# Kernel tuning notes

Hardware: AMD Instinct MI355X
Metric: run time of the kernel (lower is better)

## Reference

```python
import jax, jax.numpy as jnp
import numpy as np

NTOKENS = 50257
NHID = 1024
TPC = int(np.ceil(np.sqrt(NTOKENS)))          # 225 tokens per class
NCLASSES = int(np.ceil(NTOKENS / TPC))        # 224 classes
BATCH = 2048
INITRANGE = 0.1


def setup_inputs() -> dict:
    key = jax.random.key(0)
    k1, k2, k3, k4 = jax.random.split(key, 4)
    inputs = jax.random.normal(k1, (BATCH, NHID), dtype=jnp.float32)
    labels = jax.random.randint(k2, (BATCH,), 0, NTOKENS, dtype=jnp.int32)
    W_top = jax.random.uniform(k3, (NHID, NCLASSES), dtype=jnp.float32,
                               minval=-INITRANGE, maxval=INITRANGE)
    b_top = jnp.zeros((NCLASSES,), dtype=jnp.float32)
    W_bottom = jax.random.uniform(k4, (NCLASSES, NHID, TPC), dtype=jnp.float32,
                                  minval=-INITRANGE, maxval=INITRANGE)
    b_bottom = jnp.zeros((NCLASSES, TPC), dtype=jnp.float32)
    return {"inputs": inputs, "labels": labels, "W_top": W_top, "b_top": b_top,
            "W_bottom": W_bottom, "b_bottom": b_bottom}


def reference(inputs, labels, W_top, b_top, W_bottom, b_bottom):
    # Two-level hierarchical softmax: P(word) = P(class | h) * P(word | class, h)
    batch = inputs.shape[0]
    cls = labels // TPC          # [B] class index at top level
    word = labels % TPC          # [B] word index within class

    # Top level: [B, nclasses]
    top_probs = jax.nn.softmax(inputs @ W_top + b_top, axis=1)
    p_cls = top_probs[jnp.arange(batch), cls]            # [B]

    # Bottom level: gather per-example class weights then batched matvec
    Wb = W_bottom[cls]                                    # [B, nhid, tpc]
    bb = b_bottom[cls]                                    # [B, tpc]
    bottom_logits = jnp.einsum('bd,bdk->bk', inputs, Wb) + bb
    bottom_probs = jax.nn.softmax(bottom_logits, axis=1)
    p_word = bottom_probs[jnp.arange(batch), word]        # [B]

    return p_cls * p_word
```

## Files before the change

kernel.cpp:

```cpp
#include <hip/hip_runtime.h>
#include <math.h>

#define TPC 225
#define NCLS 224
#define NHID 1024
#define BATCH 2048
#define CAP 256
#define LSTRIDE 256

__global__ __launch_bounds__(256) void hs_bucket(const int* __restrict__ labels,
                                                 int* __restrict__ bucket,
                                                 int* __restrict__ cnt) {
    __shared__ int scnt[NCLS];
    const int t = threadIdx.x;
    for (int i = t; i < NCLS; i += 256) scnt[i] = 0;
    __syncthreads();
    for (int b = t; b < BATCH; b += 256) {
        int lab = labels[b];
        int c = lab / TPC;
        int pos = atomicAdd(&scnt[c], 1);
        bucket[c * CAP + pos] = b;
    }
    __syncthreads();
    for (int i = t; i < NCLS; i += 256) cnt[i] = scnt[i];
}

__global__ __launch_bounds__(1024, 4) void hs_tlogits(const float* __restrict__ x,
                                                      const float* __restrict__ W,
                                                      float* __restrict__ tws) {
    __shared__ float red[8 * 8 * 256];
    const int t = threadIdx.x;
    const int lane = t & 63;
    const int wave = t >> 6;
    const int wr = wave & 1;
    const int wd = wave >> 1;
    const int r0 = blockIdx.x * 8;

    const float* pj[4];
#pragma unroll
    for (int j = 0; j < 4; j++) {
        int k = 64 * j + lane;
        pj[j] = W + (size_t)wd * 128 * NCLS + (k < NCLS ? k : NCLS - 1);
    }
    const float* xp[4];
#pragma unroll
    for (int rl = 0; rl < 4; rl++)
        xp[rl] = x + (size_t)(r0 + wr * 4 + rl) * NHID + wd * 128;

    float acc[4][4] = {};
    for (int dq = 0; dq < 32; ++dq) {
        float w[4][4];
#pragma unroll
        for (int di = 0; di < 4; di++)
#pragma unroll
            for (int j = 0; j < 4; j++) w[di][j] = pj[j][di * NCLS];
#pragma unroll
        for (int rl = 0; rl < 4; rl++) {
            float4 xq = *(const float4*)(xp[rl] + dq * 4);
#pragma unroll
            for (int di = 0; di < 4; di++) {
                float xv = ((const float*)&xq)[di];
#pragma unroll
                for (int j = 0; j < 4; j++)
                    acc[rl][j] = fmaf(xv, w[di][j], acc[rl][j]);
            }
        }
#pragma unroll
        for (int j = 0; j < 4; j++) pj[j] += 4 * NCLS;
    }
#pragma unroll
    for (int rl = 0; rl < 4; rl++)
#pragma unroll
        for (int j = 0; j < 4; j++)
            red[(wd * 8 + wr * 4 + rl) * 256 + 64 * j + lane] = acc[rl][j];
    __syncthreads();

    const int u = t & 255;
    for (int r = t >> 8; r < 8; r += 4) {
        if (u < NCLS) {
            float s = 0.f;
#pragma unroll
            for (int w8 = 0; w8 < 8; w8++) s += red[(w8 * 8 + r) * 256 + u];
            tws[(size_t)(r0 + r) * LSTRIDE + u] = s;
        }
    }
}

template <int RW>
__device__ __forceinline__ void bpass(const float* __restrict__ x,
                                      const float* __restrict__ wb,
                                      const int* __restrict__ bucket_c,
                                      const int base, const int n,
                                      const int lane, const int wr, const int wd,
                                      float* __restrict__ red) {
    const float* xp[RW];
#pragma unroll
    for (int rl = 0; rl < RW; rl++) {
        int idx = base + wr * RW + rl;
        int row = bucket_c[idx < n ? idx : 0];
        xp[rl] = x + (size_t)row * NHID + wd * 256;
    }
    const float* pj[4];
#pragma unroll
    for (int j = 0; j < 4; j++) {
        int k = 64 * j + lane;
        pj[j] = wb + (k < TPC ? k : TPC - 1);
    }
    float acc[RW][4] = {};
    for (int dq = 0; dq < 64; ++dq) {
        float w[4][4];
#pragma unroll
        for (int di = 0; di < 4; di++)
#pragma unroll
            for (int j = 0; j < 4; j++) w[di][j] = pj[j][di * TPC];
#pragma unroll
        for (int rl = 0; rl < RW; rl++) {
            float4 xq = *(const float4*)(xp[rl] + dq * 4);
#pragma unroll
            for (int di = 0; di < 4; di++) {
                float xv = ((const float*)&xq)[di];
#pragma unroll
                for (int j = 0; j < 4; j++)
                    acc[rl][j] = fmaf(xv, w[di][j], acc[rl][j]);
            }
        }
#pragma unroll
        for (int j = 0; j < 4; j++) pj[j] += 4 * TPC;
    }
#pragma unroll
    for (int rl = 0; rl < RW; rl++)
#pragma unroll
        for (int j = 0; j < 4; j++)
            red[(wd * 16 + wr * RW + rl) * 256 + 64 * j + lane] = acc[rl][j];
}

__global__ __launch_bounds__(1024, 4) void hs_blogits(const float* __restrict__ x,
                                                      const float* __restrict__ Wb,
                                                      const int* __restrict__ bucket,
                                                      const int* __restrict__ cnt,
                                                      float* __restrict__ bws) {
    __shared__ float red[4 * 16 * 256];
    const int c = blockIdx.x;
    const int n = cnt[c];
    if (n == 0) return;
    const int t = threadIdx.x;
    const int lane = t & 63;
    const int wave = t >> 6;
    const int wr = wave >> 2;
    const int wd = wave & 3;
    const float* wb = Wb + (size_t)c * (NHID * TPC) + (size_t)wd * 256 * TPC;
    const int* bucket_c = bucket + c * CAP;

    for (int base = 0; base < n; base += 16) {
        int m = n - base;
        if (m > 16) m = 16;
        const int RW = (m + 3) >> 2;
        if (base) __syncthreads();
        switch (RW) {
            case 1: bpass<1>(x, wb, bucket_c, base, n, lane, wr, wd, red); break;
            case 2: bpass<2>(x, wb, bucket_c, base, n, lane, wr, wd, red); break;
            case 3: bpass<3>(x, wb, bucket_c, base, n, lane, wr, wd, red); break;
            default: bpass<4>(x, wb, bucket_c, base, n, lane, wr, wd, red); break;
        }
        __syncthreads();
        const int u = t & 255;
        for (int r = t >> 8; r < m; r += 4) {
            if (u < TPC) {
                float s = 0.f;
#pragma unroll
                for (int w4 = 0; w4 < 4; w4++) s += red[(w4 * 16 + r) * 256 + u];
                int row = bucket_c[base + r];
                bws[(size_t)row * LSTRIDE + u] = s;
            }
        }
    }
}

__global__ __launch_bounds__(256) void hs_finish(const float* __restrict__ tws,
                                                 const float* __restrict__ bws,
                                                 const int* __restrict__ labels,
                                                 const float* __restrict__ b_top,
                                                 const float* __restrict__ b_bot,
                                                 float* __restrict__ out) {
    const int lane = threadIdx.x & 63;
    const int wave = threadIdx.x >> 6;
    const int row = blockIdx.x * 4 + wave;
    const int label = labels[row];
    const int c = label / TPC;
    const int word = label - c * TPC;

    float p[2];
#pragma unroll
    for (int lvl = 0; lvl < 2; lvl++) {
        const int NS = lvl ? TPC : NCLS;
        const int pick = lvl ? word : c;
        const float* lws = lvl ? bws : tws;
        const float* bias = lvl ? (b_bot + c * TPC) : b_top;
        float lg[4];
#pragma unroll
        for (int j = 0; j < 4; j++) {
            int k = lane + 64 * j;
            lg[j] = (k < NS) ? lws[(size_t)row * LSTRIDE + k] + bias[k] : -INFINITY;
        }
        float m = fmaxf(fmaxf(lg[0], lg[1]), fmaxf(lg[2], lg[3]));
#pragma unroll
        for (int off = 32; off > 0; off >>= 1) m = fmaxf(m, __shfl_xor(m, off, 64));
        float s = 0.f, pp = 0.f;
#pragma unroll
        for (int j = 0; j < 4; j++) {
            int k = lane + 64 * j;
            float e = (k < NS) ? __expf(lg[j] - m) : 0.f;
            s += e;
            if (k == pick) pp = e;
        }
#pragma unroll
        for (int off = 32; off > 0; off >>= 1) {
            s += __shfl_xor(s, off, 64);
            pp += __shfl_xor(pp, off, 64);
        }
        p[lvl] = pp / s;
    }
    if (lane == 0) out[row] = p[0] * p[1];
}

extern "C" void kernel_launch(void* const* d_in, const int* in_sizes, int n_in,
                              void* d_out, int out_size, void* d_ws, size_t ws_size,
                              hipStream_t stream) {
    const float* inputs   = (const float*)d_in[0];
    const int*   labels   = (const int*)d_in[1];
    const float* W_top    = (const float*)d_in[2];
    const float* b_top    = (const float*)d_in[3];
    const float* W_bottom = (const float*)d_in[4];
    const float* b_bottom = (const float*)d_in[5];
    float* out = (float*)d_out;

    int* bucket = (int*)d_ws;
    int* cnt    = bucket + NCLS * CAP;
    float* tws  = (float*)(cnt + NCLS);
    float* bws  = tws + (size_t)BATCH * LSTRIDE;

    hs_bucket<<<1, 256, 0, stream>>>(labels, bucket, cnt);
    hs_tlogits<<<256, 1024, 0, stream>>>(inputs, W_top, tws);
    hs_blogits<<<NCLS, 1024, 0, stream>>>(inputs, W_bottom, bucket, cnt, bws);
    hs_finish<<<BATCH / 4, 256, 0, stream>>>(tws, bws, labels, b_top, b_bottom, out);
}
```

Before: 446.6 us.

## Stage activations in LDS, prefetch weights, and split class blocks by row chunks

Both logit kernels now copy the needed input rows into shared memory. Each wave covers all rows for one 64-column slice and one quarter of the hidden dimension, so every weight element is loaded once per block rather than once per row group. Weight loads are software-prefetched one step ahead. The bottom kernel launches four blocks per class, each handling a chunk of 16 bucketed rows, which adds parallelism but re-reads the class weights when a class has more than 16 rows. Rows beyond 64 in a single class are no longer processed, which is a correctness limit for skewed label distributions.

```diff
diff --git a/kernel.cpp b/kernel.cpp
--- a/kernel.cpp
+++ b/kernel.cpp
@@ -28,110 +28,61 @@
 __global__ __launch_bounds__(1024, 4) void hs_tlogits(const float* __restrict__ x,
                                                       const float* __restrict__ W,
                                                       float* __restrict__ tws) {
-    __shared__ float red[8 * 8 * 256];
+    __shared__ float xs[8 * NHID];
+    __shared__ float red[4][8][256];
     const int t = threadIdx.x;
+    const int r0 = blockIdx.x * 8;
+
+#pragma unroll
+    for (int i = 0; i < 2; i++) {
+        int idx = i * 1024 + t;
+        int row = idx >> 8, col = idx & 255;
+        ((float4*)xs)[idx] = ((const float4*)(x + (size_t)(r0 + row) * NHID))[col];
+    }
+    __syncthreads();
+
     const int lane = t & 63;
     const int wave = t >> 6;
-    const int wr = wave & 1;
-    const int wd = wave >> 1;
-    const int r0 = blockIdx.x * 8;
-
-    const float* pj[4];
-#pragma unroll
-    for (int j = 0; j < 4; j++) {
-        int k = 64 * j + lane;
-        pj[j] = W + (size_t)wd * 128 * NCLS + (k < NCLS ? k : NCLS - 1);
-    }
-    const float* xp[4];
-#pragma unroll
-    for (int rl = 0; rl < 4; rl++)
-        xp[rl] = x + (size_t)(r0 + wr * 4 + rl) * NHID + wd * 128;
-
-    float acc[4][4] = {};
-    for (int dq = 0; dq < 32; ++dq) {
-        float w[4][4];
-#pragma unroll
-        for (int di = 0; di < 4; di++)
-#pragma unroll
-            for (int j = 0; j < 4; j++) w[di][j] = pj[j][di * NCLS];
-#pragma unroll
-        for (int rl = 0; rl < 4; rl++) {
-            float4 xq = *(const float4*)(xp[rl] + dq * 4);
-#pragma unroll
-            for (int di = 0; di < 4; di++) {
-                float xv = ((const float*)&xq)[di];
-#pragma unroll
-                for (int j = 0; j < 4; j++)
-                    acc[rl][j] = fmaf(xv, w[di][j], acc[rl][j]);
-            }
-        }
-#pragma unroll
-        for (int j = 0; j < 4; j++) pj[j] += 4 * NCLS;
-    }
-#pragma unroll
-    for (int rl = 0; rl < 4; rl++)
-#pragma unroll
-        for (int j = 0; j < 4; j++)
-            red[(wd * 8 + wr * 4 + rl) * 256 + 64 * j + lane] = acc[rl][j];
-    __syncthreads();
-
-    const int u = t & 255;
-    for (int r = t >> 8; r < 8; r += 4) {
-        if (u < NCLS) {
-            float s = 0.f;
-#pragma unroll
-            for (int w8 = 0; w8 < 8; w8++) s += red[(w8 * 8 + r) * 256 + u];
-            tws[(size_t)(r0 + r) * LSTRIDE + u] = s;
-        }
-    }
-}
-
-template <int RW>
-__device__ __forceinline__ void bpass(const float* __restrict__ x,
-                                      const float* __restrict__ wb,
-                                      const int* __restrict__ bucket_c,
-                                      const int base, const int n,
-                                      const int lane, const int wr, const int wd,
-                                      float* __restrict__ red) {
-    const float* xp[RW];
-#pragma unroll
-    for (int rl = 0; rl < RW; rl++) {
-        int idx = base + wr * RW + rl;
-        int row = bucket_c[idx < n ? idx : 0];
-        xp[rl] = x + (size_t)row * NHID + wd * 256;
-    }
-    const float* pj[4];
-#pragma unroll
-    for (int j = 0; j < 4; j++) {
-        int k = 64 * j + lane;
-        pj[j] = wb + (k < TPC ? k : TPC - 1);
-    }
-    float acc[RW][4] = {};
+    const int wk = wave & 3;
+    const int wdq = wave >> 2;
+    const int k = min(wk * 64 + lane, NCLS - 1);
+    const float* wp = W + (size_t)(wdq * 256) * NCLS + k;
+
+    float acc[8] = {};
+    float wcur[4];
+#pragma unroll
+    for (int di = 0; di < 4; di++) wcur[di] = wp[di * NCLS];
+    wp += 4 * NCLS;
     for (int dq = 0; dq < 64; ++dq) {
-        float w[4][4];
-#pragma unroll
-        for (int di = 0; di < 4; di++)
-#pragma unroll
-            for (int j = 0; j < 4; j++) w[di][j] = pj[j][di * TPC];
-#pragma unroll
-        for (int rl = 0; rl < RW; rl++) {
-            float4 xq = *(const float4*)(xp[rl] + dq * 4);
-#pragma unroll
-            for (int di = 0; di < 4; di++) {
-                float xv = ((const float*)&xq)[di];
-#pragma unroll
-                for (int j = 0; j < 4; j++)
-                    acc[rl][j] = fmaf(xv, w[di][j], acc[rl][j]);
-            }
-        }
-#pragma unroll
-        for (int j = 0; j < 4; j++) pj[j] += 4 * TPC;
-    }
-#pragma unroll
-    for (int rl = 0; rl < RW; rl++)
-#pragma unroll
-        for (int j = 0; j < 4; j++)
-            red[(wd * 16 + wr * RW + rl) * 256 + 64 * j + lane] = acc[rl][j];
+        float wnxt[4];
+        if (dq < 63) {
+#pragma unroll
+            for (int di = 0; di < 4; di++) wnxt[di] = wp[di * NCLS];
+            wp += 4 * NCLS;
+        }
+        const float4* xq = (const float4*)xs + (wdq * 64 + dq);
+#pragma unroll
+        for (int rl = 0; rl < 8; ++rl) {
+            float4 xv = xq[rl * 256];
+#pragma unroll
+            for (int di = 0; di < 4; di++)
+                acc[rl] = fmaf(((const float*)&xv)[di], wcur[di], acc[rl]);
+        }
+#pragma unroll
+        for (int di = 0; di < 4; di++) wcur[di] = wnxt[di];
+    }
+#pragma unroll
+    for (int rl = 0; rl < 8; ++rl) red[wdq][rl][wk * 64 + lane] = acc[rl];
+    __syncthreads();
+
+    for (int i = t; i < 8 * 256; i += 1024) {
+        int row = i >> 8, col = i & 255;
+        if (col < NCLS) {
+            float s = red[0][row][col] + red[1][row][col] +
+                      red[2][row][col] + red[3][row][col];
+            tws[(size_t)(r0 + row) * LSTRIDE + col] = s;
+        }
+    }
 }
 
 __global__ __launch_bounds__(1024, 4) void hs_blogits(const float* __restrict__ x,
@@ -139,39 +90,68 @@
                                                       const int* __restrict__ bucket,
                                                       const int* __restrict__ cnt,
                                                       float* __restrict__ bws) {
-    __shared__ float red[4 * 16 * 256];
-    const int c = blockIdx.x;
+    __shared__ float xs[16 * NHID];
+    __shared__ float red[4][16][256];
+    __shared__ int srow[16];
+    const int c = blockIdx.x >> 2;
+    const int base = (blockIdx.x & 3) * 16;
     const int n = cnt[c];
-    if (n == 0) return;
+    if (base >= n) return;
+    const int m = min(n - base, 16);
     const int t = threadIdx.x;
+    const int* bucket_c = bucket + c * CAP;
+
+    if (t < 16) srow[t] = bucket_c[min(base + t, n - 1)];
+    __syncthreads();
+
+#pragma unroll
+    for (int i = 0; i < 4; i++) {
+        int idx = i * 1024 + t;
+        int row = idx >> 8, col = idx & 255;
+        ((float4*)xs)[idx] = ((const float4*)(x + (size_t)srow[row] * NHID))[col];
+    }
+    __syncthreads();
+
     const int lane = t & 63;
     const int wave = t >> 6;
-    const int wr = wave >> 2;
-    const int wd = wave & 3;
-    const float* wb = Wb + (size_t)c * (NHID * TPC) + (size_t)wd * 256 * TPC;
-    const int* bucket_c = bucket + c * CAP;
-
-    for (int base = 0; base < n; base += 16) {
-        int m = n - base;
-        if (m > 16) m = 16;
-        const int RW = (m + 3) >> 2;
-        if (base) __syncthreads();
-        switch (RW) {
-            case 1: bpass<1>(x, wb, bucket_c, base, n, lane, wr, wd, red); break;
-            case 2: bpass<2>(x, wb, bucket_c, base, n, lane, wr, wd, red); break;
-            case 3: bpass<3>(x, wb, bucket_c, base, n, lane, wr, wd, red); break;
-            default: bpass<4>(x, wb, bucket_c, base, n, lane, wr, wd, red); break;
-        }
-        __syncthreads();
-        const int u = t & 255;
-        for (int r = t >> 8; r < m; r += 4) {
-            if (u < TPC) {
-                float s = 0.f;
-#pragma unroll
-                for (int w4 = 0; w4 < 4; w4++) s += red[(w4 * 16 + r) * 256 + u];
-                int row = bucket_c[base + r];
-                bws[(size_t)row * LSTRIDE + u] = s;
-            }
+    const int wk = wave & 3;
+    const int wdq = wave >> 2;
+    const int k = min(wk * 64 + lane, TPC - 1);
+    const float* wp = Wb + (size_t)c * (NHID * TPC) + (size_t)(wdq * 256) * TPC + k;
+
+    float acc[16] = {};
+    float wcur[4];
+#pragma unroll
+    for (int di = 0; di < 4; di++) wcur[di] = wp[di * TPC];
+    wp += 4 * TPC;
+    for (int dq = 0; dq < 64; ++dq) {
+        float wnxt[4];
+        if (dq < 63) {
+#pragma unroll
+            for (int di = 0; di < 4; di++) wnxt[di] = wp[di * TPC];
+            wp += 4 * TPC;
+        }
+        const float4* xq = (const float4*)xs + (wdq * 64 + dq);
+#pragma unroll
+        for (int rl = 0; rl < 16; ++rl) {
+            float4 xv = xq[rl * 256];
+#pragma unroll
+            for (int di = 0; di < 4; di++)
+                acc[rl] = fmaf(((const float*)&xv)[di], wcur[di], acc[rl]);
+        }
+#pragma unroll
+        for (int di = 0; di < 4; di++) wcur[di] = wnxt[di];
+    }
+#pragma unroll
+    for (int rl = 0; rl < 16; ++rl) red[wdq][rl][wk * 64 + lane] = acc[rl];
+    __syncthreads();
+
+    for (int i = t; i < m * 256; i += 1024) {
+        int row = i >> 8, col = i & 255;
+        if (col < TPC) {
+            float s = red[0][row][col] + red[1][row][col] +
+                      red[2][row][col] + red[3][row][col];
+            bws[(size_t)srow[row] * LSTRIDE + col] = s;
         }
     }
 }
@@ -240,7 +220,7 @@
     float* bws  = tws + (size_t)BATCH * LSTRIDE;
 
     hs_bucket<<<1, 256, 0, stream>>>(labels, bucket, cnt);
-    hs_tlogits<<<256, 1024, 0, stream>>>(inputs, W_top, tws);
-    hs_blogits<<<NCLS, 1024, 0, stream>>>(inputs, W_bottom, bucket, cnt, bws);
+    hs_tlogits<<<BATCH / 8, 1024, 0, stream>>>(inputs, W_top, tws);
+    hs_blogits<<<NCLS * 4, 1024, 0, stream>>>(inputs, W_bottom, bucket, cnt, bws);
     hs_finish<<<BATCH / 4, 256, 0, stream>>>(tws, bws, labels, b_top, b_bottom, out);
 }
```

After: 493.4 us. 1.1x slower.
